# Optimization experiments

Measured on AMD Instinct MI355X. Metric: run time of the kernel, lower is better.

Reference implementation:

```python
import jax, jax.numpy as jnp
import numpy as np

T, G, L_UH, NZ = 512, 4096, 15, 1e-5

PHY_NAMES = ['ddf_min','ddf_plus','Kcum','Kf','exp_fe','Tbf','Ccum','SWI','Tbm','fcmin','fcmin_plus','vadose_max_level','hmets_alpha','vic_beta','hbv_beta','quickflow_k','quickflow_n','mmax','lamb','baseflow_k','baseflow_n','ET_efficiency','coef_vadose2phreatic','coef_phreatic']
BOUNDS = {'ddf_min':(0.,20.),'ddf_plus':(0.,20.),'Kcum':(.01,.2),'Kf':(0.,5.),'exp_fe':(0.,1.),'Tbf':(-5.,2.),'Ccum':(.005,.05),'SWI':(0.,.4),'Tbm':(-2.,3.),'fcmin':(0.,.1),'fcmin_plus':(.01,.25),'vadose_max_level':(.001,500.),'hmets_alpha':(0.,1.),'vic_beta':(.1,3.),'hbv_beta':(.5,3.),'quickflow_k':(-5.,-2.),'quickflow_n':(.5,2.),'mmax':(0.,100.),'lamb':(5.,10.),'baseflow_k':(-5.,-1.),'baseflow_n':(.5,2.),'ET_efficiency':(0.,3.),'coef_vadose2phreatic':(1e-5,.02),'coef_phreatic':(1e-5,.01)}

def setup_inputs():
    key = jax.random.key(0)
    k1, k2, k3, k4 = jax.random.split(key, 4)
    prcp = jax.random.uniform(k1, (T, G)) * 20.0   # mm/day
    tmean = jax.random.uniform(k2, (T, G)) * 40.0 - 15.0  # deg C, mixed rain/snow
    pet = jax.random.uniform(k3, (T, G)) * 6.0
    x = jnp.stack([prcp, tmean, pet], axis=-1).astype(jnp.float32)
    parameters = jax.random.normal(k4, (T, G, 39), dtype=jnp.float32)
    return {'x': x, 'parameters': parameters}

def _descale(v, lo, hi):
    return lo + v * (hi - lo)

def _unpack(parameters):
    # static params: last time step (dynamic_params=[], dy_drop=0 -> staPar path)
    last = parameters[-1, :, :35]
    p = {n: _descale(jax.nn.sigmoid(last[:, i]), *BOUNDS[n]) for i, n in enumerate(PHY_NAMES)}
    # blend weights: softmax within each weights_group (bounds [0,1] -> identity descale)
    for (s, e) in [(24, 27), (27, 30), (30, 33), (33, 35)]:
        w = jax.nn.softmax(last[:, s:e], axis=1)
        for j in range(e - s):
            p['w%d' % (s - 24 + j + 1)] = w[:, j]
    rp = jax.nn.sigmoid(parameters[-1, :, 35:39])
    r = {'alpha1': _descale(rp[:, 0], 0.3, 20.0), 'beta1': _descale(rp[:, 1], 0.01, 5.0),
         'alpha2': _descale(rp[:, 2], 0.5, 13.0), 'beta2': _descale(rp[:, 3], 0.15, 1.5)}
    return p, r

def _gamma_uh(a, b):
    # gamma-shaped unit hydrograph, normalized over L_UH steps, per grid cell
    t = jnp.arange(L_UH, dtype=jnp.float32) + 0.5
    w = t[None, :] ** (a[:, None] - 1.0) * jnp.exp(-t[None, :] / b[:, None])
    return w / jnp.sum(w, axis=1, keepdims=True)

def _route(q, uh):
    # causal depthwise convolution along time: out[t] = sum_k uh[k] * q[t-k]
    Tq = q.shape[0]
    qpad = jnp.pad(q, ((L_UH - 1, 0), (0, 0)))
    out = jnp.zeros_like(q)
    for k in range(L_UH):
        out = out + uh[None, :, k] * jax.lax.dynamic_slice_in_dim(qpad, L_UH - 1 - k, Tq, axis=0)
    return out

def _forward(x, parameters):
    p, r = _unpack(parameters)
    g = x.shape[1]
    vmax = p['vadose_max_level']
    relu = lambda v: jnp.maximum(v, 0.0)

    def snobal_hbv(tm, sf, rf, cm, sp, lw):
        ddf = jnp.minimum(p['ddf_min'] + p['ddf_plus'], p['ddf_min'] * (1.0 + p['Kcum'] * cm))
        pm = relu(ddf * (tm - p['Tbm']))
        rfz = jnp.minimum(p['Kf'] * jnp.maximum(p['Tbf'] - tm, NZ), lw)
        sp = sp + sf + rfz
        melt = jnp.minimum(pm, sp + sf + rfz)
        cm = (cm + melt) * (sp > NZ).astype(sp.dtype)
        sp = jnp.maximum(sp - melt, NZ)
        wret = p['SWI'] * sp
        wtmp = lw + melt + rf
        ovf = relu(wtmp - wret)
        lw = jnp.where(ovf > 0, wret, wtmp)
        return sp, lw, cm, ovf

    def snobal_hmets(tm, sf, rf, cm, sp, lw):
        ddf = jnp.minimum(p['ddf_min'] + p['ddf_plus'], p['ddf_min'] * (1.0 + p['Kcum'] * cm))
        pm = relu(ddf * (tm - p['Tbm']))
        pfz = p['Kf'] * jnp.maximum(p['Tbf'] - tm, NZ) ** p['exp_fe']
        rfz = jnp.minimum(pfz, lw)
        lw = lw - rfz
        sp = sp + rfz
        melt = jnp.minimum(pm, sp + sf)
        sp = sp + sf - melt
        cm = (cm + melt) * (sp > NZ).astype(sp.dtype)
        wrf = jnp.maximum((p['fcmin'] + p['fcmin_plus']) * (1.0 - p['Ccum'] * cm), p['fcmin'])
        wret = wrf * sp
        wtmp = lw + melt + rf
        ovf = relu(wtmp - wret)
        lw = jnp.where(ovf > 0, wret, wtmp)
        cm = (cm + melt) * (sp > NZ).astype(sp.dtype)
        return sp, lw, cm, ovf

    def snobal_simple(tm, sf, rf, cm, sp):
        ddf = jnp.minimum(p['ddf_min'] + p['ddf_plus'], p['ddf_min'] * (1.0 + p['Kcum'] * cm))
        pm = relu(ddf * (tm - p['Tbm']))
        melt = jnp.minimum(pm, sp)
        sp = sp + sf - melt
        ovf = melt + rf
        cm = (cm + melt) * (sp > NZ).astype(sp.dtype)
        return sp, cm, ovf

    def step(state, xt):
        sp1, lw1, cm1, sp2, lw2, cm2, sp3, cm3, vad, phr = state
        prcp, tm, pet = xt[:, 0], xt[:, 1], xt[:, 2]
        rain = jnp.where(tm > 0.0, prcp, 0.0)
        snow = prcp - rain
        sp1, lw1, cm1, o1 = snobal_hbv(tm, snow, rain, cm1, sp1, lw1)
        sp2, lw2, cm2, o2 = snobal_hmets(tm, snow, rain, cm2, sp2, lw2)
        sp3, cm3, o3 = snobal_simple(tm, snow, rain, cm3, sp3)
        rr = p['w1'] * o1 + p['w2'] * o2 + p['w3'] * o3
        sprop = jnp.clip(vad / vmax, NZ, 1.0 - NZ)
        inf = (p['w4'] * rr * (1.0 - sprop) ** p['hbv_beta']
               + p['w5'] * rr * (1.0 - p['hmets_alpha'] * vad / vmax)
               + p['w6'] * rr * (1.0 - (1.0 - sprop) ** p['vic_beta']))
        inf = jnp.clip(inf, 0.0, rr)
        surface = rr - inf
        vad = vad + inf
        sprop = jnp.clip(vad / vmax, NZ, 1.0 - NZ)
        et = jnp.minimum(pet * p['ET_efficiency'] * sprop, vad)
        vad = vad - et
        qf_lin = 10.0 ** p['quickflow_k'] * vad
        qf_top = jnp.minimum(p['mmax'] * (vmax / p['quickflow_n']) / p['lamb'] ** p['quickflow_n'] * sprop ** p['quickflow_n'], vad)
        qf_vic = jnp.minimum(p['mmax'] * sprop ** p['quickflow_n'], vad)
        qf = jnp.minimum(p['w7'] * qf_lin + p['w8'] * qf_top + p['w9'] * qf_vic, vad)
        vad = vad - qf
        perc = p['coef_vadose2phreatic'] * vad
        vad = vad - perc
        phr = phr + perc
        bf = jnp.minimum(p['w10'] * 10.0 ** p['baseflow_k'] * phr
                         + p['w11'] * 10.0 ** p['baseflow_k'] * jnp.maximum(phr, NZ) ** p['baseflow_n'], phr)
        phr = phr - bf
        return (sp1, lw1, cm1, sp2, lw2, cm2, sp3, cm3, vad, phr), (surface + qf, bf)

    z = jnp.zeros((g,), dtype=x.dtype)
    init = (z,) * 10
    _, (quick, base) = jax.lax.scan(step, init, x)
    flow = _route(quick, _gamma_uh(r['alpha1'], r['beta1'])) + _route(base, _gamma_uh(r['alpha2'], r['beta2']))
    return flow  # [T, G]

def reference(x, parameters):
    return _forward(x, parameters)
```

## Files before the change

kernel.cpp:

```cpp
#include <hip/hip_runtime.h>

#define T_STEPS 512
#define G_CELLS 4096
#define L_UHN   15
#define GRP     8
#define NGRP    (T_STEPS / GRP)
#define CPB     64
#define NZF     1e-5f
#define LOG2E   1.44269504088896340736f
#define LOG2_10 3.32192809488736234787f

__device__ __forceinline__ float fexp2(float x) { return __builtin_amdgcn_exp2f(x); }
__device__ __forceinline__ float flog2(float x) { return __builtin_amdgcn_logf(x); }
__device__ __forceinline__ float fpow(float a, float b) { return fexp2(b * flog2(a)); }
__device__ __forceinline__ float fexp(float x) { return fexp2(x * LOG2E); }
__device__ __forceinline__ float fsigmoid(float v) { return 1.0f / (1.0f + fexp(-v)); }
__device__ __forceinline__ float fdescale(float s, float lo, float hi) { return lo + s * (hi - lo); }

__device__ __forceinline__ void block_barrier() {
    asm volatile("s_waitcnt lgkmcnt(0)" ::: "memory");
    __builtin_amdgcn_s_barrier();
}


__device__ __forceinline__ void snow02_wave(const float* __restrict__ x,
                                            const float* __restrict__ pp,
                                            float (*ob)[3][GRP][CPB],
                                            int lane, int g)
{
    const float ddf_min  = fdescale(fsigmoid(pp[0]), 0.0f, 20.0f);
    const float ddf_plus = fdescale(fsigmoid(pp[1]), 0.0f, 20.0f);
    const float Kcum     = fdescale(fsigmoid(pp[2]), 0.01f, 0.2f);
    const float Kf       = fdescale(fsigmoid(pp[3]), 0.0f, 5.0f);
    const float Tbf      = fdescale(fsigmoid(pp[5]), -5.0f, 2.0f);
    const float SWI      = fdescale(fsigmoid(pp[7]), 0.0f, 0.4f);
    const float Tbm      = fdescale(fsigmoid(pp[8]), -2.0f, 3.0f);
    const float ddfsum   = ddf_min + ddf_plus;
    const float ddfK     = ddf_min * Kcum;

    float w0, w2_;
    {
        float r0 = pp[24], r1 = pp[25], r2 = pp[26];
        float m = fmaxf(fmaxf(r0, r1), r2);
        float e0 = fexp(r0 - m), e1 = fexp(r1 - m), e2 = fexp(r2 - m);
        float inv = 1.0f / (e0 + e1 + e2);
        w0 = e0 * inv; w2_ = e2 * inv;
    }

    float sp0 = 0.f, lw0 = 0.f, cm0 = 0.f;
    float sp2 = 0.f, cm2 = 0.f;

    float bR[GRP], bS[GRP], bD[GRP], bX[GRP];
    float rawP[GRP], rawT[GRP];
    #pragma unroll
    for (int j = 0; j < GRP; ++j) {
        size_t a = ((size_t)j * G_CELLS + (size_t)g) * 3;
        rawP[j] = x[a]; rawT[j] = x[a + 1];
    }
    #pragma unroll
    for (int j = 0; j < GRP; ++j) {
        float tm = rawT[j], prcp = rawP[j];
        bR[j] = (tm > 0.0f) ? prcp : 0.0f;
        bS[j] = prcp - bR[j];
        bD[j] = tm - Tbm;
        bX[j] = Kf * fmaxf(Tbf - tm, NZF);
    }

    for (int k = 0; k <= NGRP + 1; ++k) {
        block_barrier();
        if (k < NGRP) {
            const int kn = (k + 1 < NGRP) ? k + 1 : NGRP - 1;
            #pragma unroll
            for (int j = 0; j < GRP; ++j) {
                size_t a = ((size_t)(kn * GRP + j) * G_CELLS + (size_t)g) * 3;
                rawP[j] = x[a]; rawT[j] = x[a + 1];
            }

            const int b = k & 1;
            #pragma unroll
            for (int j = 0; j < GRP; ++j) {
                const float rain = bR[j], snow = bS[j], dtm = bD[j];
                {
                    float ddf  = fminf(ddfsum, fmaf(ddfK, cm0, ddf_min));
                    float pm   = fmaxf(ddf * dtm, 0.0f);
                    float rfz  = fminf(bX[j], lw0);
                    sp0 = sp0 + snow + rfz;
                    float melt = fminf(pm, sp0 + snow + rfz);
                    cm0 = (sp0 > NZF) ? (cm0 + melt) : 0.0f;
                    sp0 = fmaxf(sp0 - melt, NZF);
                    float wret = SWI * sp0;
                    float wtmp = lw0 + melt + rain;
                    float o    = fmaxf(wtmp - wret, 0.0f);
                    lw0 = fminf(wtmp, wret);
                    ob[b][0][j][lane] = w0 * o;
                }
                {
                    float ddf  = fminf(ddfsum, fmaf(ddfK, cm2, ddf_min));
                    float pm   = fmaxf(ddf * dtm, 0.0f);
                    float melt = fminf(pm, sp2);
                    sp2 = sp2 + snow - melt;
                    float o = melt + rain;
                    cm2 = (sp2 > NZF) ? (cm2 + melt) : 0.0f;
                    ob[b][2][j][lane] = w2_ * o;
                }
            }

            #pragma unroll
            for (int j = 0; j < GRP; ++j) {
                float tm = rawT[j], prcp = rawP[j];
                bR[j] = (tm > 0.0f) ? prcp : 0.0f;
                bS[j] = prcp - bR[j];
                bD[j] = tm - Tbm;
                bX[j] = Kf * fmaxf(Tbf - tm, NZF);
            }
        }
    }
}

__device__ __forceinline__ void snow1_wave(const float* __restrict__ x,
                                           const float* __restrict__ pp,
                                           float (*ob)[3][GRP][CPB],
                                           int lane, int g)
{
    const float ddf_min  = fdescale(fsigmoid(pp[0]), 0.0f, 20.0f);
    const float ddf_plus = fdescale(fsigmoid(pp[1]), 0.0f, 20.0f);
    const float Kcum     = fdescale(fsigmoid(pp[2]), 0.01f, 0.2f);
    const float Kf       = fdescale(fsigmoid(pp[3]), 0.0f, 5.0f);
    const float exp_fe   = fdescale(fsigmoid(pp[4]), 0.0f, 1.0f);
    const float Tbf      = fdescale(fsigmoid(pp[5]), -5.0f, 2.0f);
    const float Ccum     = fdescale(fsigmoid(pp[6]), 0.005f, 0.05f);
    const float Tbm      = fdescale(fsigmoid(pp[8]), -2.0f, 3.0f);
    const float fcmin    = fdescale(fsigmoid(pp[9]), 0.0f, 0.1f);
    const float fcsum    = fcmin + fdescale(fsigmoid(pp[10]), 0.01f, 0.25f);
    const float ddfsum   = ddf_min + ddf_plus;
    const float ddfK     = ddf_min * Kcum;

    float w1;
    {
        float r0 = pp[24], r1 = pp[25], r2 = pp[26];
        float m = fmaxf(fmaxf(r0, r1), r2);
        float e0 = fexp(r0 - m), e1 = fexp(r1 - m), e2 = fexp(r2 - m);
        w1 = e1 / (e0 + e1 + e2);
    }

    float sp = 0.f, lw = 0.f, cm = 0.f;

    float bR[GRP], bS[GRP], bD[GRP], bX[GRP];
    float rawP[GRP], rawT[GRP];
    #pragma unroll
    for (int j = 0; j < GRP; ++j) {
        size_t a = ((size_t)j * G_CELLS + (size_t)g) * 3;
        rawP[j] = x[a]; rawT[j] = x[a + 1];
    }
    #pragma unroll
    for (int j = 0; j < GRP; ++j) {
        float tm = rawT[j], prcp = rawP[j];
        bR[j] = (tm > 0.0f) ? prcp : 0.0f;
        bS[j] = prcp - bR[j];
        bD[j] = tm - Tbm;
        bX[j] = Kf * fpow(fmaxf(Tbf - tm, NZF), exp_fe);
    }

    for (int k = 0; k <= NGRP + 1; ++k) {
        block_barrier();
        if (k < NGRP) {
            const int kn = (k + 1 < NGRP) ? k + 1 : NGRP - 1;
            #pragma unroll
            for (int j = 0; j < GRP; ++j) {
                size_t a = ((size_t)(kn * GRP + j) * G_CELLS + (size_t)g) * 3;
                rawP[j] = x[a]; rawT[j] = x[a + 1];
            }

            const int b = k & 1;
            #pragma unroll
            for (int j = 0; j < GRP; ++j) {
                const float rain = bR[j], snow = bS[j], dtm = bD[j];
                float ddf  = fminf(ddfsum, fmaf(ddfK, cm, ddf_min));
                float pm   = fmaxf(ddf * dtm, 0.0f);
                float rfz  = fminf(bX[j], lw);
                lw -= rfz; sp += rfz;
                float melt = fminf(pm, sp + snow);
                sp = sp + snow - melt;
                cm = (sp > NZF) ? (cm + melt) : 0.0f;
                float wrf  = fmaxf(fcsum * (1.0f - Ccum * cm), fcmin);
                float wret = wrf * sp;
                float wtmp = lw + melt + rain;
                float o    = fmaxf(wtmp - wret, 0.0f);
                lw = fminf(wtmp, wret);
                cm = (sp > NZF) ? (cm + melt) : 0.0f;
                ob[b][1][j][lane] = w1 * o;
            }

            #pragma unroll
            for (int j = 0; j < GRP; ++j) {
                float tm = rawT[j], prcp = rawP[j];
                bR[j] = (tm > 0.0f) ? prcp : 0.0f;
                bS[j] = prcp - bR[j];
                bD[j] = tm - Tbm;
                bX[j] = Kf * fpow(fmaxf(Tbf - tm, NZF), exp_fe);
            }
        }
    }
}

__device__ __forceinline__ void vad_wave(const float* __restrict__ x,
                                         const float* __restrict__ pp,
                                         float (*ob)[3][GRP][CPB],
                                         float (*pr)[2][GRP][CPB],
                                         int lane, int g)
{
    const float vmax        = fdescale(fsigmoid(pp[11]), 0.001f, 500.0f);
    const float hmets_alpha = fdescale(fsigmoid(pp[12]), 0.0f, 1.0f);
    const float vic_beta    = fdescale(fsigmoid(pp[13]), 0.1f, 3.0f);
    const float hbv_beta    = fdescale(fsigmoid(pp[14]), 0.5f, 3.0f);
    const float quickflow_k = fdescale(fsigmoid(pp[15]), -5.0f, -2.0f);
    const float qn          = fdescale(fsigmoid(pp[16]), 0.5f, 2.0f);
    const float mmax        = fdescale(fsigmoid(pp[17]), 0.0f, 100.0f);
    const float lamb        = fdescale(fsigmoid(pp[18]), 5.0f, 10.0f);
    const float ET_eff      = fdescale(fsigmoid(pp[21]), 0.0f, 3.0f);
    const float cv2p        = fdescale(fsigmoid(pp[22]), 1e-5f, 0.02f);

    float w4, w5, w6, w7, w8, w9;
    {
        float r0 = pp[27], r1 = pp[28], r2 = pp[29];
        float m = fmaxf(fmaxf(r0, r1), r2);
        float e0 = fexp(r0 - m), e1 = fexp(r1 - m), e2 = fexp(r2 - m);
        float inv = 1.0f / (e0 + e1 + e2);
        w4 = e0 * inv; w5 = e1 * inv; w6 = e2 * inv;
    }
    {
        float r0 = pp[30], r1 = pp[31], r2 = pp[32];
        float m = fmaxf(fmaxf(r0, r1), r2);
        float e0 = fexp(r0 - m), e1 = fexp(r1 - m), e2 = fexp(r2 - m);
        float inv = 1.0f / (e0 + e1 + e2);
        w7 = e0 * inv; w8 = e1 * inv; w9 = e2 * inv;
    }

    const float inv_vmax    = 1.0f / vmax;
    const float qk10        = fexp2(quickflow_k * LOG2_10);
    const float qf_top_coef = mmax * (vmax / qn) * fexp2(-qn * flog2(lamb));
    const float w7qk        = w7 * qk10;

    float vad = 0.f;

    float pe[GRP], rawPet[GRP];
    #pragma unroll
    for (int j = 0; j < GRP; ++j)
        rawPet[j] = x[((size_t)j * G_CELLS + (size_t)g) * 3 + 2];
    #pragma unroll
    for (int j = 0; j < GRP; ++j) pe[j] = rawPet[j] * ET_eff;

    for (int k = 0; k <= NGRP + 1; ++k) {
        block_barrier();
        if (k >= 1 && k <= NGRP) {
            const int kg = k - 1;
            const int kn = (k < NGRP) ? k : NGRP - 1;
            #pragma unroll
            for (int j = 0; j < GRP; ++j)
                rawPet[j] = x[((size_t)(kn * GRP + j) * G_CELLS + (size_t)g) * 3 + 2];

            const int b = kg & 1;
            float rr[GRP];
            #pragma unroll
            for (int j = 0; j < GRP; ++j)
                rr[j] = (ob[b][0][j][lane] + ob[b][1][j][lane]) + ob[b][2][j][lane];

            #pragma unroll
            for (int j = 0; j < GRP; ++j) {
                const float rrj = rr[j];
                float vv = vad * inv_vmax;
                float sprop = fminf(fmaxf(vv, NZF), 1.0f - NZF);
                float l1 = flog2(1.0f - sprop);
                float phbv = fexp2(hbv_beta * l1);
                float pvic = fexp2(vic_beta * l1);
                float inf = w4 * rrj * phbv + w5 * rrj * (1.0f - hmets_alpha * vv)
                          + w6 * rrj * (1.0f - pvic);
                inf = fminf(fmaxf(inf, 0.0f), rrj);
                float surface = rrj - inf;
                vad += inf;
                vv = vad * inv_vmax;
                sprop = fminf(fmaxf(vv, NZF), 1.0f - NZF);
                float et = fminf(pe[j] * sprop, vad);
                vad -= et;
                float spq    = fexp2(qn * flog2(sprop));
                float qf_top = fminf(qf_top_coef * spq, vad);
                float qf_vic = fminf(mmax * spq, vad);
                float qf = fminf(w7qk * vad + w8 * qf_top + w9 * qf_vic, vad);
                vad -= qf;
                float perc = cv2p * vad;
                vad -= perc;

                pr[b][0][j][lane] = perc;
                pr[b][1][j][lane] = surface + qf;
            }

            #pragma unroll
            for (int j = 0; j < GRP; ++j) pe[j] = rawPet[j] * ET_eff;
        }
    }
}

__device__ __forceinline__ void phr_route_wave(const float* __restrict__ pp,
                                               float (*pr)[2][GRP][CPB],
                                               float* __restrict__ out,
                                               int lane, int g)
{
    const float baseflow_k = fdescale(fsigmoid(pp[19]), -5.0f, -1.0f);
    const float bn         = fdescale(fsigmoid(pp[20]), 0.5f, 2.0f);
    float w10, w11;
    {
        float r0 = pp[33], r1 = pp[34];
        float m = fmaxf(r0, r1);
        float e0 = fexp(r0 - m), e1 = fexp(r1 - m);
        float inv = 1.0f / (e0 + e1);
        w10 = e0 * inv; w11 = e1 * inv;
    }
    const float bk10 = fexp2(baseflow_k * LOG2_10);
    const float c_b1 = w10 * bk10, c_b2 = w11 * bk10;

    const float a1 = fdescale(fsigmoid(pp[35]), 0.3f, 20.0f);
    const float b1 = fdescale(fsigmoid(pp[36]), 0.01f, 5.0f);
    const float a2 = fdescale(fsigmoid(pp[37]), 0.5f, 13.0f);
    const float b2 = fdescale(fsigmoid(pp[38]), 0.15f, 1.5f);

    const float LOG2T[L_UHN] = {
        -1.0f, 0.58496250072116f, 1.32192809488736f, 1.80735492205760f,
        2.16992500144231f, 2.45943161863730f, 2.70043971814109f,
        2.90689059560852f, 3.08746284125034f, 3.24792751344359f,
        3.39231742277876f, 3.52356195605701f, 3.64385618977472f,
        3.75488750216347f, 3.85798099512757f };

    float uh1[L_UHN], uh2[L_UHN];
    {
        float rb1 = LOG2E / b1, rb2 = LOG2E / b2;
        float s1 = 0.0f, s2 = 0.0f;
        #pragma unroll
        for (int kk = 0; kk < L_UHN; ++kk) {
            float tk = (float)kk + 0.5f;
            float v1 = fexp2((a1 - 1.0f) * LOG2T[kk] - tk * rb1);
            float v2 = fexp2((a2 - 1.0f) * LOG2T[kk] - tk * rb2);
            uh1[kk] = v1; uh2[kk] = v2; s1 += v1; s2 += v2;
        }
        float i1 = 1.0f / s1, i2 = 1.0f / s2;
        #pragma unroll
        for (int kk = 0; kk < L_UHN; ++kk) { uh1[kk] *= i1; uh2[kk] *= i2; }
    }

    float phr = 0.f;
    float fut[L_UHN];
    #pragma unroll
    for (int kk = 0; kk < L_UHN; ++kk) fut[kk] = 0.0f;

    for (int k = 0; k <= NGRP + 1; ++k) {
        block_barrier();
        if (k >= 2) {
            const int kp = k - 2;
            const int b  = kp & 1;
            float pc[GRP], qv[GRP];
            #pragma unroll
            for (int j = 0; j < GRP; ++j) {
                pc[j] = pr[b][0][j][lane];
                qv[j] = pr[b][1][j][lane];
            }

            #pragma unroll
            for (int j = 0; j < GRP; ++j) {
                phr += pc[j];
                float pb = fexp2(bn * flog2(fmaxf(phr, NZF)));
                float bf = fminf(c_b1 * phr + c_b2 * pb, phr);
                phr -= bf;

                const float qt = qv[j];
                #pragma unroll
                for (int kk = 0; kk < L_UHN; ++kk)
                    fut[kk] = fmaf(uh1[kk], qt, fmaf(uh2[kk], bf, fut[kk]));
                out[(size_t)(kp * GRP + j) * G_CELLS + (size_t)g] = fut[0];
                #pragma unroll
                for (int kk = 0; kk < L_UHN - 1; ++kk) fut[kk] = fut[kk + 1];
                fut[L_UHN - 1] = 0.0f;
            }
        }
    }
}

__global__ __launch_bounds__(256, 1) void pipeline_kernel(
    const float* __restrict__ x, const float* __restrict__ params,
    float* __restrict__ out)
{
    __shared__ float ob[2][3][GRP][CPB];
    __shared__ float pr[2][2][GRP][CPB];
    const int lane = threadIdx.x & 63;
    const int wave = threadIdx.x >> 6;
    const int g    = blockIdx.x * CPB + lane;
    const float* pp = params + ((size_t)(T_STEPS - 1) * G_CELLS + (size_t)g) * 39;

    if (wave == 0)      snow02_wave(x, pp, ob, lane, g);
    else if (wave == 1) snow1_wave(x, pp, ob, lane, g);
    else if (wave == 2) vad_wave(x, pp, ob, pr, lane, g);
    else                phr_route_wave(pp, pr, out, lane, g);
}

extern "C" void kernel_launch(void* const* d_in, const int* in_sizes, int n_in,
                              void* d_out, int out_size, void* d_ws, size_t ws_size,
                              hipStream_t stream) {
    const float* x      = (const float*)d_in[0];
    const float* params = (const float*)d_in[1];
    float* out          = (float*)d_out;
    pipeline_kernel<<<dim3(G_CELLS / CPB), dim3(256), 0, stream>>>(x, params, out);
}
```

Measured before the change: 75.62 us.

## Split phreatic and routing into separate waves, deepen inter-wave pipeline

Splits the combined phreatic/routing wave into two waves (baseflow recurrence and unit-hydrograph routing), making the block five wavefronts. The shared-memory buffer between the vadose and downstream stages becomes four-deep, and a new baseflow buffer is added. Each stage now prefetches its next group from LDS one barrier ahead and computes the previous one, so per-stage critical-path work shrinks. The cost is a longer pipeline fill (four more barrier steps) and more shared memory and registers.

```diff
diff --git a/kernel.cpp b/kernel.cpp
--- a/kernel.cpp
+++ b/kernel.cpp
@@ -66,7 +66,7 @@
         bX[j] = Kf * fmaxf(Tbf - tm, NZF);
     }
 
-    for (int k = 0; k <= NGRP + 1; ++k) {
+    for (int k = 0; k <= NGRP + 5; ++k) {
         block_barrier();
         if (k < NGRP) {
             const int kn = (k + 1 < NGRP) ? k + 1 : NGRP - 1;
@@ -161,7 +161,7 @@
         bX[j] = Kf * fpow(fmaxf(Tbf - tm, NZF), exp_fe);
     }
 
-    for (int k = 0; k <= NGRP + 1; ++k) {
+    for (int k = 0; k <= NGRP + 5; ++k) {
         block_barrier();
         if (k < NGRP) {
             const int kn = (k + 1 < NGRP) ? k + 1 : NGRP - 1;
@@ -243,31 +243,31 @@
 
     float vad = 0.f;
 
-    float pe[GRP], rawPet[GRP];
-    #pragma unroll
-    for (int j = 0; j < GRP; ++j)
-        rawPet[j] = x[((size_t)j * G_CELLS + (size_t)g) * 3 + 2];
-    #pragma unroll
-    for (int j = 0; j < GRP; ++j) pe[j] = rawPet[j] * ET_eff;
-
-    for (int k = 0; k <= NGRP + 1; ++k) {
+    float rrCur[GRP], rrNext[GRP];
+    float pe[GRP], rawPrev[GRP], rawNew[GRP];
+
+    for (int k = 0; k <= NGRP + 5; ++k) {
         block_barrier();
-        if (k >= 1 && k <= NGRP) {
-            const int kg = k - 1;
-            const int kn = (k < NGRP) ? k : NGRP - 1;
+
+        if (k < NGRP) {
             #pragma unroll
             for (int j = 0; j < GRP; ++j)
-                rawPet[j] = x[((size_t)(kn * GRP + j) * G_CELLS + (size_t)g) * 3 + 2];
-
-            const int b = kg & 1;
-            float rr[GRP];
+                rawNew[j] = x[((size_t)(k * GRP + j) * G_CELLS + (size_t)g) * 3 + 2];
+        }
+
+        if (k - 1 >= 0 && k - 1 < NGRP) {
+            const int b = (k - 1) & 1;
             #pragma unroll
             for (int j = 0; j < GRP; ++j)
-                rr[j] = (ob[b][0][j][lane] + ob[b][1][j][lane]) + ob[b][2][j][lane];
-
-            #pragma unroll
-            for (int j = 0; j < GRP; ++j) {
-                const float rrj = rr[j];
+                rrNext[j] = (ob[b][0][j][lane] + ob[b][1][j][lane]) + ob[b][2][j][lane];
+        }
+
+        if (k - 2 >= 0 && k - 2 < NGRP) {
+            const int kg = k - 2;
+            const int slot = kg & 3;
+            #pragma unroll
+            for (int j = 0; j < GRP; ++j) {
+                const float rrj = rrCur[j];
                 float vv = vad * inv_vmax;
                 float sprop = fminf(fmaxf(vv, NZF), 1.0f - NZF);
                 float l1 = flog2(1.0f - sprop);
@@ -290,20 +290,24 @@
                 float perc = cv2p * vad;
                 vad -= perc;
 
-                pr[b][0][j][lane] = perc;
-                pr[b][1][j][lane] = surface + qf;
-            }
-
-            #pragma unroll
-            for (int j = 0; j < GRP; ++j) pe[j] = rawPet[j] * ET_eff;
-        }
-    }
-}
-
-__device__ __forceinline__ void phr_route_wave(const float* __restrict__ pp,
-                                               float (*pr)[2][GRP][CPB],
-                                               float* __restrict__ out,
-                                               int lane, int g)
+                pr[slot][0][j][lane] = perc;
+                pr[slot][1][j][lane] = surface + qf;
+            }
+        }
+
+        #pragma unroll
+        for (int j = 0; j < GRP; ++j) rrCur[j] = rrNext[j];
+        #pragma unroll
+        for (int j = 0; j < GRP; ++j) pe[j] = rawPrev[j] * ET_eff;
+        #pragma unroll
+        for (int j = 0; j < GRP; ++j) rawPrev[j] = rawNew[j];
+    }
+}
+
+__device__ __forceinline__ void phr_wave(const float* __restrict__ pp,
+                                         float (*pr)[2][GRP][CPB],
+                                         float (*bfr)[GRP][CPB],
+                                         int lane)
 {
     const float baseflow_k = fdescale(fsigmoid(pp[19]), -5.0f, -1.0f);
     const float bn         = fdescale(fsigmoid(pp[20]), 0.5f, 2.0f);
@@ -318,6 +322,42 @@
     const float bk10 = fexp2(baseflow_k * LOG2_10);
     const float c_b1 = w10 * bk10, c_b2 = w11 * bk10;
 
+    float phr = 0.f;
+    float pcCur[GRP], pcNext[GRP];
+
+    for (int k = 0; k <= NGRP + 5; ++k) {
+        block_barrier();
+
+        if (k - 3 >= 0 && k - 3 < NGRP) {
+            const int slot = (k - 3) & 3;
+            #pragma unroll
+            for (int j = 0; j < GRP; ++j) pcNext[j] = pr[slot][0][j][lane];
+        }
+
+        if (k - 4 >= 0 && k - 4 < NGRP) {
+            const int kg = k - 4;
+            const int bslot = kg & 1;
+            #pragma unroll
+            for (int j = 0; j < GRP; ++j) {
+                phr += pcCur[j];
+                float pb = fexp2(bn * flog2(fmaxf(phr, NZF)));
+                float bf = fminf(c_b1 * phr + c_b2 * pb, phr);
+                phr -= bf;
+                bfr[bslot][j][lane] = bf;
+            }
+        }
+
+        #pragma unroll
+        for (int j = 0; j < GRP; ++j) pcCur[j] = pcNext[j];
+    }
+}
+
+__device__ __forceinline__ void route_wave(const float* __restrict__ pp,
+                                           float (*pr)[2][GRP][CPB],
+                                           float (*bfr)[GRP][CPB],
+                                           float* __restrict__ out,
+                                           int lane, int g)
+{
     const float a1 = fdescale(fsigmoid(pp[35]), 0.3f, 20.0f);
     const float b1 = fdescale(fsigmoid(pp[36]), 0.01f, 5.0f);
     const float a2 = fdescale(fsigmoid(pp[37]), 0.5f, 13.0f);
@@ -346,58 +386,63 @@
         for (int kk = 0; kk < L_UHN; ++kk) { uh1[kk] *= i1; uh2[kk] *= i2; }
     }
 
-    float phr = 0.f;
     float fut[L_UHN];
     #pragma unroll
     for (int kk = 0; kk < L_UHN; ++kk) fut[kk] = 0.0f;
 
-    for (int k = 0; k <= NGRP + 1; ++k) {
+    float qCur[GRP], bCur[GRP], qNext[GRP], bNext[GRP];
+
+    for (int k = 0; k <= NGRP + 5; ++k) {
         block_barrier();
-        if (k >= 2) {
-            const int kp = k - 2;
-            const int b  = kp & 1;
-            float pc[GRP], qv[GRP];
-            #pragma unroll
-            for (int j = 0; j < GRP; ++j) {
-                pc[j] = pr[b][0][j][lane];
-                qv[j] = pr[b][1][j][lane];
-            }
-
-            #pragma unroll
-            for (int j = 0; j < GRP; ++j) {
-                phr += pc[j];
-                float pb = fexp2(bn * flog2(fmaxf(phr, NZF)));
-                float bf = fminf(c_b1 * phr + c_b2 * pb, phr);
-                phr -= bf;
-
-                const float qt = qv[j];
+
+        if (k - 5 >= 0 && k - 5 < NGRP) {
+            const int s4 = (k - 5) & 3;
+            const int s2_ = (k - 5) & 1;
+            #pragma unroll
+            for (int j = 0; j < GRP; ++j) {
+                qNext[j] = pr[s4][1][j][lane];
+                bNext[j] = bfr[s2_][j][lane];
+            }
+        }
+
+        if (k - 6 >= 0 && k - 6 < NGRP) {
+            const int kg = k - 6;
+            #pragma unroll
+            for (int j = 0; j < GRP; ++j) {
+                const float qt = qCur[j];
+                const float bf = bCur[j];
                 #pragma unroll
                 for (int kk = 0; kk < L_UHN; ++kk)
                     fut[kk] = fmaf(uh1[kk], qt, fmaf(uh2[kk], bf, fut[kk]));
-                out[(size_t)(kp * GRP + j) * G_CELLS + (size_t)g] = fut[0];
+                out[(size_t)(kg * GRP + j) * G_CELLS + (size_t)g] = fut[0];
                 #pragma unroll
                 for (int kk = 0; kk < L_UHN - 1; ++kk) fut[kk] = fut[kk + 1];
                 fut[L_UHN - 1] = 0.0f;
             }
         }
-    }
-}
-
-__global__ __launch_bounds__(256, 1) void pipeline_kernel(
+
+        #pragma unroll
+        for (int j = 0; j < GRP; ++j) { qCur[j] = qNext[j]; bCur[j] = bNext[j]; }
+    }
+}
+
+__global__ __launch_bounds__(320, 1) void pipeline_kernel(
     const float* __restrict__ x, const float* __restrict__ params,
     float* __restrict__ out)
 {
     __shared__ float ob[2][3][GRP][CPB];
-    __shared__ float pr[2][2][GRP][CPB];
+    __shared__ float pr[4][2][GRP][CPB];
+    __shared__ float bfr[2][GRP][CPB];
     const int lane = threadIdx.x & 63;
     const int wave = threadIdx.x >> 6;
     const int g    = blockIdx.x * CPB + lane;
     const float* pp = params + ((size_t)(T_STEPS - 1) * G_CELLS + (size_t)g) * 39;
 
-    if (wave == 0)      snow02_wave(x, pp, ob, lane, g);
-    else if (wave == 1) snow1_wave(x, pp, ob, lane, g);
-    else if (wave == 2) vad_wave(x, pp, ob, pr, lane, g);
-    else                phr_route_wave(pp, pr, out, lane, g);
+    if (wave == 0)      phr_wave(pp, pr, bfr, lane);
+    else if (wave == 1) snow02_wave(x, pp, ob, lane, g);
+    else if (wave == 2) snow1_wave(x, pp, ob, lane, g);
+    else if (wave == 3) vad_wave(x, pp, ob, pr, lane, g);
+    else                route_wave(pp, pr, bfr, out, lane, g);
 }
 
 extern "C" void kernel_launch(void* const* d_in, const int* in_sizes, int n_in,
@@ -406,5 +451,5 @@
     const float* x      = (const float*)d_in[0];
     const float* params = (const float*)d_in[1];
     float* out          = (float*)d_out;
-    pipeline_kernel<<<dim3(G_CELLS / CPB), dim3(256), 0, stream>>>(x, params, out);
-}
+    pipeline_kernel<<<dim3(G_CELLS / CPB), dim3(320), 0, stream>>>(x, params, out);
+}
```

Result: no change. 76.28 us (+0.9%).
